# Optimization experiments

Hardware: AMD Instinct MI355X
Metric: run time of the kernel (lower is better)

## Reference

```python
import jax, jax.numpy as jnp
import numpy as np

NUM_HEADS = 12
SCALE = 0.125  # (C // num_heads) ** -0.5 = 64 ** -0.5


def setup_inputs() -> dict:
    key = jax.random.key(0)
    k1, k2, k3, k4, k5 = jax.random.split(key, 5)
    B, N, C = 8, 1024, 768
    x = jax.random.normal(k1, (B, N, C), dtype=jnp.float32)
    qkv_w = jax.random.normal(k2, (3 * C, C), dtype=jnp.float32) * (C ** -0.5)
    qkv_b = jax.random.normal(k3, (3 * C,), dtype=jnp.float32) * 0.02
    proj_w = jax.random.normal(k4, (C, C), dtype=jnp.float32) * (C ** -0.5)
    proj_b = jax.random.normal(k5, (C,), dtype=jnp.float32) * 0.02
    return {"x": x, "qkv_w": qkv_w, "qkv_b": qkv_b,
            "proj_w": proj_w, "proj_b": proj_b, "H": 32, "W": 32}


def reference(x, qkv_w, qkv_b, proj_w, proj_b, H, W):
    B, N, C = x.shape
    hd = C // NUM_HEADS
    # qkv: [B, N, 3C] -> [3, B, heads, N, hd]
    qkv = (x @ qkv_w.T + qkv_b).reshape(B, N, 3, NUM_HEADS, hd)
    qkv = jnp.transpose(qkv, (2, 0, 3, 1, 4))
    q, k, v = qkv[0], qkv[1], qkv[2]
    # attention scores [B, heads, N, N]
    attn = jnp.einsum('bhnd,bhmd->bhnm', q, k) * SCALE
    attn = jax.nn.softmax(attn, axis=-1)
    # attn_drop / proj_drop are identity in eval mode
    out = jnp.einsum('bhnm,bhmd->bhnd', attn, v)
    out = jnp.transpose(out, (0, 2, 1, 3)).reshape(B, N, C)
    out = out @ proj_w.T + proj_b
    return out
```

## Files before the change

kernel.cpp:

```cpp
#include <hip/hip_runtime.h>
#include <math.h>

#define NSEQ  1024
#define CDIM  768
#define NH    12
#define HD    64
#define QS    6291456
#define EXPC  0.18033688011112042f

typedef __bf16 bf16x8 __attribute__((ext_vector_type(8)));
typedef float  f32x4  __attribute__((ext_vector_type(4)));

__device__ __forceinline__ unsigned short f2bf(float f) {
    union { float f; unsigned u; } v; v.f = f;
    unsigned r = v.u + 0x7FFFu + ((v.u >> 16) & 1u);
    return (unsigned short)(r >> 16);
}

#if __has_builtin(__builtin_amdgcn_cvt_pk_bf16_f32)
typedef __bf16 bf16x2 __attribute__((ext_vector_type(2)));
__device__ __forceinline__ void store_p4(unsigned short* pr, int row16,
                                         float p0, float p1, float p2, float p3) {
    union { bf16x2 v; unsigned u; } a, b;
    a.v = __builtin_amdgcn_cvt_pk_bf16_f32(p0, p1);
    b.v = __builtin_amdgcn_cvt_pk_bf16_f32(p2, p3);
    pr[row16]      = (unsigned short)(a.u);
    pr[16 + row16] = (unsigned short)(a.u >> 16);
    pr[32 + row16] = (unsigned short)(b.u);
    pr[48 + row16] = (unsigned short)(b.u >> 16);
}
#else
__device__ __forceinline__ void store_p4(unsigned short* pr, int row16,
                                         float p0, float p1, float p2, float p3) {
    pr[row16]      = f2bf(p0);
    pr[16 + row16] = f2bf(p1);
    pr[32 + row16] = f2bf(p2);
    pr[48 + row16] = f2bf(p3);
}
#endif

__device__ __forceinline__ void gld_lds16(const unsigned short* g, unsigned short* l) {
    __builtin_amdgcn_global_load_lds(
        (const __attribute__((address_space(1))) void*)g,
        (__attribute__((address_space(3))) void*)l, 16, 0, 0);
}

__global__ __launch_bounds__(256) void cvt_all(const float* __restrict__ x,
                                               const float* __restrict__ w1,
                                               const float* __restrict__ w2,
                                               unsigned short* __restrict__ xb,
                                               unsigned short* __restrict__ w1b,
                                               unsigned short* __restrict__ w2b,
                                               int n0, int n1, int n2) {
    int i = (blockIdx.x * 256 + threadIdx.x) * 4;
    const float* s; unsigned short* d; int off;
    if (i < n0)           { s = x;  d = xb;  off = i; }
    else if (i < n0 + n1) { s = w1; d = w1b; off = i - n0; }
    else if (i < n0 + n1 + n2) { s = w2; d = w2b; off = i - n0 - n1; }
    else return;
    float4 v = *(const float4*)(s + off);
    ushort4 o;
    o.x = f2bf(v.x); o.y = f2bf(v.y); o.z = f2bf(v.z); o.w = f2bf(v.w);
    *(ushort4*)(d + off) = o;
}

template <int MODE>
__global__ __launch_bounds__(256) void mfma_gemm_bt(const unsigned short* __restrict__ A,
                                                    const unsigned short* __restrict__ Bw,
                                                    const float* __restrict__ bias,
                                                    void* __restrict__ outp,
                                                    int M, int N, int K) {
    __shared__ unsigned short smem[2 * 128 * 32];
    unsigned short* As = smem;
    unsigned short* Bs = smem + 128 * 32;

    const int tid = threadIdx.x;
    const int wave = tid >> 6, lane = tid & 63;
    const int row16 = lane & 15, quad = lane >> 4;
    const int wm = (wave >> 1) * 64, wn = (wave & 1) * 64;
    const int m0 = blockIdx.x * 128, n0 = blockIdx.y * 128;

    f32x4 acc[4][4];
#pragma unroll
    for (int i = 0; i < 4; ++i)
#pragma unroll
        for (int j = 0; j < 4; ++j) acc[i][j] = (f32x4){0.f, 0.f, 0.f, 0.f};

    for (int k0 = 0; k0 < K; k0 += 32) {
        __syncthreads();
#pragma unroll
        for (int i = 0; i < 2; ++i) {
            const int flat = (tid + i * 256) * 8;
            const int row = flat >> 5, col = flat & 31;
            gld_lds16(&A[(size_t)(m0 + row) * K + k0 + col], &As[i * 2048 + wave * 512]);
            gld_lds16(&Bw[(size_t)(n0 + row) * K + k0 + col], &Bs[i * 2048 + wave * 512]);
        }
        __syncthreads();
        bf16x8 af[4], bfr[4];
#pragma unroll
        for (int mt = 0; mt < 4; ++mt)
            af[mt] = *(const bf16x8*)&As[(wm + mt * 16 + row16) * 32 + quad * 8];
#pragma unroll
        for (int nt = 0; nt < 4; ++nt)
            bfr[nt] = *(const bf16x8*)&Bs[(wn + nt * 16 + row16) * 32 + quad * 8];
#pragma unroll
        for (int mt = 0; mt < 4; ++mt)
#pragma unroll
            for (int nt = 0; nt < 4; ++nt)
                acc[mt][nt] = __builtin_amdgcn_mfma_f32_16x16x32_bf16(af[mt], bfr[nt], acc[mt][nt], 0, 0, 0);
    }

    float bias4[4];
#pragma unroll
    for (int nt = 0; nt < 4; ++nt) bias4[nt] = bias[n0 + wn + nt * 16 + row16];

    if (MODE == 0) {
#pragma unroll
        for (int mt = 0; mt < 4; ++mt)
#pragma unroll
            for (int nt = 0; nt < 4; ++nt)
#pragma unroll
                for (int r = 0; r < 4; ++r) {
                    int grow = m0 + wm + mt * 16 + quad * 4 + r;
                    int gcol = n0 + wn + nt * 16 + row16;
                    ((float*)outp)[(size_t)grow * N + gcol] = acc[mt][nt][r] + bias4[nt];
                }
    } else {
        unsigned short* qkvb = (unsigned short*)outp;
#pragma unroll
        for (int p = 0; p < 2; ++p) {
            __syncthreads();
            if ((wave >> 1) == p) {
#pragma unroll
                for (int mt = 0; mt < 4; ++mt)
#pragma unroll
                    for (int nt = 0; nt < 4; ++nt)
#pragma unroll
                        for (int r = 0; r < 4; ++r)
                            smem[(mt * 16 + quad * 4 + r) * 128 + wn + nt * 16 + row16] =
                                f2bf(acc[mt][nt][r] + bias4[nt]);
            }
            __syncthreads();
#pragma unroll
            for (int i = 0; i < 4; ++i) {
                int u4 = i * 256 + tid;
                int row = u4 >> 4;
                int c8 = u4 & 15;
                int grow = m0 + p * 64 + row;
                int gcol = n0 + c8 * 8;
                int t = gcol / CDIM;
                int rr = gcol - t * CDIM;
                int h = rr >> 6, d = rr & 63;
                int b = grow >> 10, n = grow & 1023;
                *(uint4*)&qkvb[(size_t)t * QS + ((((size_t)b * NH + h) << 10) + n) * 64 + d] =
                    *(const uint4*)&smem[row * 128 + c8 * 8];
            }
        }
    }
}

__global__ __launch_bounds__(256, 4) void attn_mfma(const unsigned short* __restrict__ qkv,
                                                    unsigned short* __restrict__ abuf) {
    __shared__ unsigned short Ks[64 * 72];
    __shared__ unsigned short Vt[64 * 72];
    __shared__ unsigned short Ps[4][32 * 72];

    const int tid = threadIdx.x;
    const int wave = tid >> 6, lane = tid & 63;
    const int row16 = lane & 15, quad = lane >> 4;
    const int bid = blockIdx.x;
    const int xcd = bid & 7;
    const int local = bid >> 3;
    const int bh = xcd * 12 + (local >> 3);
    const int qt = local & 7;

    const unsigned short* Qg = qkv + (size_t)bh * NSEQ * HD + (size_t)qt * 128 * HD;
    const unsigned short* Kg = qkv + (size_t)QS + (size_t)bh * NSEQ * HD;
    const unsigned short* Vg = qkv + (size_t)2 * QS + (size_t)bh * NSEQ * HD;

    bf16x8 aq[2][2];
#pragma unroll
    for (int mt = 0; mt < 2; ++mt)
#pragma unroll
        for (int kst = 0; kst < 2; ++kst)
            aq[mt][kst] = *(const bf16x8*)&Qg[(size_t)(wave * 32 + mt * 16 + row16) * 64 +
                                              kst * 32 + quad * 8];

    f32x4 o[2][4];
    float l_i[2][4];
#pragma unroll
    for (int mt = 0; mt < 2; ++mt)
#pragma unroll
        for (int j = 0; j < 4; ++j) {
            o[mt][j] = (f32x4){0.f, 0.f, 0.f, 0.f};
            l_i[mt][j] = 0.f;
        }

    const int kpair = tid & 31;
    const int colc = tid >> 5;

    for (int kt = 0; kt < 16; ++kt) {
        __syncthreads();
#pragma unroll
        for (int i = 0; i < 2; ++i) {
            int flat = (tid + i * 256) * 8;
            int key = flat >> 6, col = flat & 63;
            *(uint4*)&Ks[key * 72 + col] = *(const uint4*)&Kg[(size_t)(kt * 64 + key) * 64 + col];
        }
        {
            const unsigned short* vp = &Vg[(size_t)(kt * 64 + 2 * kpair) * 64 + colc * 8];
            uint4 va = *(const uint4*)vp;
            uint4 vb = *(const uint4*)(vp + 64);
            const unsigned short* a16 = (const unsigned short*)&va;
            const unsigned short* b16 = (const unsigned short*)&vb;
            unsigned int* vt32 = (unsigned int*)Vt;
#pragma unroll
            for (int j = 0; j < 8; ++j)
                vt32[(colc * 8 + j) * 36 + kpair] =
                    (unsigned int)a16[j] | ((unsigned int)b16[j] << 16);
        }
        __syncthreads();

        f32x4 s[2][4];
#pragma unroll
        for (int mt = 0; mt < 2; ++mt)
#pragma unroll
            for (int nt = 0; nt < 4; ++nt) s[mt][nt] = (f32x4){0.f, 0.f, 0.f, 0.f};
#pragma unroll
        for (int kst = 0; kst < 2; ++kst) {
            bf16x8 bk[4];
#pragma unroll
            for (int nt = 0; nt < 4; ++nt)
                bk[nt] = *(const bf16x8*)&Ks[(nt * 16 + row16) * 72 + kst * 32 + quad * 8];
#pragma unroll
            for (int mt = 0; mt < 2; ++mt)
#pragma unroll
                for (int nt = 0; nt < 4; ++nt)
                    s[mt][nt] = __builtin_amdgcn_mfma_f32_16x16x32_bf16(aq[mt][kst], bk[nt], s[mt][nt], 0, 0, 0);
        }

#pragma unroll
        for (int mt = 0; mt < 2; ++mt)
#pragma unroll
            for (int r = 0; r < 4; ++r) {
                float p0 = __builtin_amdgcn_exp2f(s[mt][0][r] * EXPC);
                float p1 = __builtin_amdgcn_exp2f(s[mt][1][r] * EXPC);
                float p2 = __builtin_amdgcn_exp2f(s[mt][2][r] * EXPC);
                float p3 = __builtin_amdgcn_exp2f(s[mt][3][r] * EXPC);
                l_i[mt][r] += (p0 + p1) + (p2 + p3);
                store_p4(&Ps[wave][(mt * 16 + quad * 4 + r) * 72], row16, p0, p1, p2, p3);
            }

#pragma unroll
        for (int kst = 0; kst < 2; ++kst) {
            bf16x8 ap[2], bv[4];
#pragma unroll
            for (int mt = 0; mt < 2; ++mt)
                ap[mt] = *(const bf16x8*)&Ps[wave][(mt * 16 + row16) * 72 + kst * 32 + quad * 8];
#pragma unroll
            for (int dt = 0; dt < 4; ++dt)
                bv[dt] = *(const bf16x8*)&Vt[(dt * 16 + row16) * 72 + kst * 32 + quad * 8];
#pragma unroll
            for (int mt = 0; mt < 2; ++mt)
#pragma unroll
                for (int dt = 0; dt < 4; ++dt)
                    o[mt][dt] = __builtin_amdgcn_mfma_f32_16x16x32_bf16(ap[mt], bv[dt], o[mt][dt], 0, 0, 0);
        }
    }

    const int b = bh / NH, h = bh - b * NH;
#pragma unroll
    for (int mt = 0; mt < 2; ++mt)
#pragma unroll
        for (int r = 0; r < 4; ++r) {
            float l = l_i[mt][r];
            l += __shfl_xor(l, 1);
            l += __shfl_xor(l, 2);
            l += __shfl_xor(l, 4);
            l += __shfl_xor(l, 8);
            float inv = 1.f / l;
            int n = qt * 128 + wave * 32 + mt * 16 + quad * 4 + r;
            size_t base = ((size_t)(b * NSEQ + n)) * CDIM + h * HD;
#pragma unroll
            for (int dt = 0; dt < 4; ++dt)
                abuf[base + dt * 16 + row16] = f2bf(o[mt][dt][r] * inv);
        }
}

extern "C" void kernel_launch(void* const* d_in, const int* in_sizes, int n_in,
                              void* d_out, int out_size, void* d_ws, size_t ws_size,
                              hipStream_t stream) {
    const float* x      = (const float*)d_in[0];
    const float* qkv_w  = (const float*)d_in[1];
    const float* qkv_b  = (const float*)d_in[2];
    const float* proj_w = (const float*)d_in[3];
    const float* proj_b = (const float*)d_in[4];
    float* out = (float*)d_out;

    const int M = 8 * NSEQ;
    unsigned short* ws = (unsigned short*)d_ws;
    unsigned short* xb   = ws;
    unsigned short* wq   = xb + (size_t)M * CDIM;
    unsigned short* wp   = wq + (size_t)3 * CDIM * CDIM;
    unsigned short* qkvb = wp + (size_t)CDIM * CDIM;
    unsigned short* ab   = qkvb + (size_t)3 * QS;

    const int nx = M * CDIM, nq = 3 * CDIM * CDIM, np = CDIM * CDIM;
    cvt_all<<<(nx + nq + np) / 1024, 256, 0, stream>>>(x, qkv_w, proj_w, xb, wq, wp,
                                                       nx, nq, np);

    mfma_gemm_bt<1><<<dim3(M / 128, (3 * CDIM) / 128), 256, 0, stream>>>(
        xb, wq, qkv_b, qkvb, M, 3 * CDIM, CDIM);

    attn_mfma<<<dim3(8 * NH * (NSEQ / 128)), 256, 0, stream>>>(qkvb, ab);

    mfma_gemm_bt<0><<<dim3(M / 128, CDIM / 128), 256, 0, stream>>>(
        ab, wp, proj_b, out, M, CDIM, CDIM);
}
```

Measured before the change: 206.8 us.

## Double K-step in GEMM, single-pass epilogue, register-prefetch K/V in attention

The GEMM now stages a K-depth of 64 per iteration, doubling LDS to 32KB, which halves the number of barrier pairs and issues two MFMA k-steps per load. The QKV epilogue writes the whole 128x128 tile to shared memory in one pass instead of two half passes, saving barriers. The attention kernel prefetches the next K/V tile into registers right after the barrier, so global loads overlap the MFMA and softmax work. The costs are higher LDS and register use, which may lower occupancy.

```diff
diff --git a/kernel.cpp b/kernel.cpp
--- a/kernel.cpp
+++ b/kernel.cpp
@@ -70,9 +70,9 @@
                                                     const float* __restrict__ bias,
                                                     void* __restrict__ outp,
                                                     int M, int N, int K) {
-    __shared__ unsigned short smem[2 * 128 * 32];
+    __shared__ unsigned short smem[2 * 128 * 64];
     unsigned short* As = smem;
-    unsigned short* Bs = smem + 128 * 32;
+    unsigned short* Bs = smem + 128 * 64;
 
     const int tid = threadIdx.x;
     const int wave = tid >> 6, lane = tid & 63;
@@ -86,28 +86,31 @@
 #pragma unroll
         for (int j = 0; j < 4; ++j) acc[i][j] = (f32x4){0.f, 0.f, 0.f, 0.f};
 
-    for (int k0 = 0; k0 < K; k0 += 32) {
-        __syncthreads();
-#pragma unroll
-        for (int i = 0; i < 2; ++i) {
+    for (int k0 = 0; k0 < K; k0 += 64) {
+        __syncthreads();
+#pragma unroll
+        for (int i = 0; i < 4; ++i) {
             const int flat = (tid + i * 256) * 8;
-            const int row = flat >> 5, col = flat & 31;
+            const int row = flat >> 6, col = flat & 63;
             gld_lds16(&A[(size_t)(m0 + row) * K + k0 + col], &As[i * 2048 + wave * 512]);
             gld_lds16(&Bw[(size_t)(n0 + row) * K + k0 + col], &Bs[i * 2048 + wave * 512]);
         }
         __syncthreads();
-        bf16x8 af[4], bfr[4];
-#pragma unroll
-        for (int mt = 0; mt < 4; ++mt)
-            af[mt] = *(const bf16x8*)&As[(wm + mt * 16 + row16) * 32 + quad * 8];
-#pragma unroll
-        for (int nt = 0; nt < 4; ++nt)
-            bfr[nt] = *(const bf16x8*)&Bs[(wn + nt * 16 + row16) * 32 + quad * 8];
-#pragma unroll
-        for (int mt = 0; mt < 4; ++mt)
+#pragma unroll
+        for (int kst = 0; kst < 2; ++kst) {
+            bf16x8 af[4], bfr[4];
+#pragma unroll
+            for (int mt = 0; mt < 4; ++mt)
+                af[mt] = *(const bf16x8*)&As[(wm + mt * 16 + row16) * 64 + kst * 32 + quad * 8];
 #pragma unroll
             for (int nt = 0; nt < 4; ++nt)
-                acc[mt][nt] = __builtin_amdgcn_mfma_f32_16x16x32_bf16(af[mt], bfr[nt], acc[mt][nt], 0, 0, 0);
+                bfr[nt] = *(const bf16x8*)&Bs[(wn + nt * 16 + row16) * 64 + kst * 32 + quad * 8];
+#pragma unroll
+            for (int mt = 0; mt < 4; ++mt)
+#pragma unroll
+                for (int nt = 0; nt < 4; ++nt)
+                    acc[mt][nt] = __builtin_amdgcn_mfma_f32_16x16x32_bf16(af[mt], bfr[nt], acc[mt][nt], 0, 0, 0);
+        }
     }
 
     float bias4[4];
@@ -127,34 +130,29 @@
                 }
     } else {
         unsigned short* qkvb = (unsigned short*)outp;
-#pragma unroll
-        for (int p = 0; p < 2; ++p) {
-            __syncthreads();
-            if ((wave >> 1) == p) {
-#pragma unroll
-                for (int mt = 0; mt < 4; ++mt)
-#pragma unroll
-                    for (int nt = 0; nt < 4; ++nt)
-#pragma unroll
-                        for (int r = 0; r < 4; ++r)
-                            smem[(mt * 16 + quad * 4 + r) * 128 + wn + nt * 16 + row16] =
-                                f2bf(acc[mt][nt][r] + bias4[nt]);
-            }
-            __syncthreads();
-#pragma unroll
-            for (int i = 0; i < 4; ++i) {
-                int u4 = i * 256 + tid;
-                int row = u4 >> 4;
-                int c8 = u4 & 15;
-                int grow = m0 + p * 64 + row;
-                int gcol = n0 + c8 * 8;
-                int t = gcol / CDIM;
-                int rr = gcol - t * CDIM;
-                int h = rr >> 6, d = rr & 63;
-                int b = grow >> 10, n = grow & 1023;
-                *(uint4*)&qkvb[(size_t)t * QS + ((((size_t)b * NH + h) << 10) + n) * 64 + d] =
-                    *(const uint4*)&smem[row * 128 + c8 * 8];
-            }
+        __syncthreads();
+#pragma unroll
+        for (int mt = 0; mt < 4; ++mt)
+#pragma unroll
+            for (int nt = 0; nt < 4; ++nt)
+#pragma unroll
+                for (int r = 0; r < 4; ++r)
+                    smem[(wm + mt * 16 + quad * 4 + r) * 128 + wn + nt * 16 + row16] =
+                        f2bf(acc[mt][nt][r] + bias4[nt]);
+        __syncthreads();
+#pragma unroll
+        for (int i = 0; i < 8; ++i) {
+            int u4 = i * 256 + tid;
+            int row = u4 >> 4;
+            int c8 = u4 & 15;
+            int grow = m0 + row;
+            int gcol = n0 + c8 * 8;
+            int t = gcol / CDIM;
+            int rr = gcol - t * CDIM;
+            int h = rr >> 6, d = rr & 63;
+            int b = grow >> 10, n = grow & 1023;
+            *(uint4*)&qkvb[(size_t)t * QS + ((((size_t)b * NH + h) << 10) + n) * 64 + d] =
+                *(const uint4*)&smem[row * 128 + c8 * 8];
         }
     }
 }
@@ -196,21 +194,21 @@
             l_i[mt][j] = 0.f;
         }
 
+    const int krow0 = (tid * 8) >> 6,  kcol0 = (tid * 8) & 63;
+    const int krow1 = ((tid + 256) * 8) >> 6, kcol1 = ((tid + 256) * 8) & 63;
     const int kpair = tid & 31;
     const int colc = tid >> 5;
 
+    uint4 ka = *(const uint4*)&Kg[(size_t)krow0 * 64 + kcol0];
+    uint4 kb = *(const uint4*)&Kg[(size_t)krow1 * 64 + kcol1];
+    uint4 va = *(const uint4*)&Vg[(size_t)(2 * kpair) * 64 + colc * 8];
+    uint4 vb = *(const uint4*)&Vg[(size_t)(2 * kpair + 1) * 64 + colc * 8];
+
     for (int kt = 0; kt < 16; ++kt) {
         __syncthreads();
-#pragma unroll
-        for (int i = 0; i < 2; ++i) {
-            int flat = (tid + i * 256) * 8;
-            int key = flat >> 6, col = flat & 63;
-            *(uint4*)&Ks[key * 72 + col] = *(const uint4*)&Kg[(size_t)(kt * 64 + key) * 64 + col];
-        }
+        *(uint4*)&Ks[krow0 * 72 + kcol0] = ka;
+        *(uint4*)&Ks[krow1 * 72 + kcol1] = kb;
         {
-            const unsigned short* vp = &Vg[(size_t)(kt * 64 + 2 * kpair) * 64 + colc * 8];
-            uint4 va = *(const uint4*)vp;
-            uint4 vb = *(const uint4*)(vp + 64);
             const unsigned short* a16 = (const unsigned short*)&va;
             const unsigned short* b16 = (const unsigned short*)&vb;
             unsigned int* vt32 = (unsigned int*)Vt;
@@ -220,6 +218,15 @@
                     (unsigned int)a16[j] | ((unsigned int)b16[j] << 16);
         }
         __syncthreads();
+
+        if (kt < 15) {
+            const unsigned short* kn = Kg + (size_t)(kt + 1) * 64 * 64;
+            const unsigned short* vn = Vg + (size_t)(kt + 1) * 64 * 64;
+            ka = *(const uint4*)&kn[(size_t)krow0 * 64 + kcol0];
+            kb = *(const uint4*)&kn[(size_t)krow1 * 64 + kcol1];
+            va = *(const uint4*)&vn[(size_t)(2 * kpair) * 64 + colc * 8];
+            vb = *(const uint4*)&vn[(size_t)(2 * kpair + 1) * 64 + colc * 8];
+        }
 
         f32x4 s[2][4];
 #pragma unroll
```

New measurement: 219.8 us. +6.3%, slower.
